# Optimization experiments

Hardware: AMD Instinct MI355X
Metric: run time of the kernel (lower is better)

Reference implementation:

```python
import jax, jax.numpy as jnp
import numpy as np

N_SUPPORT = 32768
N_QUERY = 16384
D = 512
K = 32
U = 128
NEG_BIG = -1e30  # masked-out attention logit; all-masked class -> uniform weights == mean fallback


def setup_inputs() -> dict:
    key = jax.random.key(0)
    k1, k2, k3, k4, k5 = jax.random.split(key, 5)
    query = jax.random.normal(k1, (N_QUERY, D), dtype=jnp.float32)
    support = jax.random.normal(k2, (N_SUPPORT, D), dtype=jnp.float32)
    labels = jax.random.randint(k3, (N_SUPPORT,), 0, K, dtype=jnp.int32)
    # Xavier-normal-ish init for per-class projection V (U,D) and attention vector w (U,1)
    V = jax.random.normal(k4, (K, U, D), dtype=jnp.float32) * np.float32(np.sqrt(2.0 / (U + D)))
    w = jax.random.normal(k5, (K, U), dtype=jnp.float32) * np.float32(np.sqrt(2.0 / (U + 1)))
    return {"query_embeddings": query, "support_embeddings": support,
            "support_labels": labels, "V": V, "w": w}


def reference(query_embeddings, support_embeddings, support_labels, V, w):
    # --- attention-weighted prototypes (vectorized over classes via masked softmax) ---
    # projected[k,n,u] = tanh(V[k] @ x_n)
    projected = jnp.tanh(jnp.einsum('nd,kud->knu', support_embeddings, V))
    attn_logits = jnp.einsum('knu,ku->kn', projected, w)              # (K, N)
    mask = support_labels[None, :] == jnp.arange(K, dtype=support_labels.dtype)[:, None]
    attn_logits = jnp.where(mask, attn_logits, NEG_BIG)
    # per-class softmax over support samples; an empty class yields uniform weights,
    # i.e. prototype = mean(embeddings) -- exactly the torch fallback branch.
    attn = jax.nn.softmax(attn_logits, axis=1)                        # (K, N)
    prototypes = jnp.einsum('kn,nd->kd', attn, support_embeddings)    # (K, D)

    # --- squared-euclidean distance classification ---
    q2 = jnp.sum(query_embeddings * query_embeddings, axis=1, keepdims=True)   # (B, 1)
    p2 = jnp.sum(prototypes * prototypes, axis=1)[None, :]                     # (1, K)
    dists = q2 + p2 - 2.0 * (query_embeddings @ prototypes.T)                  # (B, K)
    return jax.nn.log_softmax(-dists, axis=1)
```

## Files before the change

kernel.cpp:

```cpp
#include <hip/hip_runtime.h>
#include <hip/hip_bf16.h>

#define N_SUPPORT 32768
#define N_QUERY   16384
#define DIM       512
#define NCLS      32
#define NU        128
#define NBLK      (N_SUPPORT / 256)

#define OFF_IDX      0
#define OFF_COUNT    131072
#define OFF_START    131200
#define OFF_M        131456
#define OFF_Z        131584
#define OFF_P2       131712
#define OFF_LOGIT    132096
#define OFF_PRAW     263168
#define OFF_PROTO    328704
#define OFF_BHIST    394240
#define OFF_BOFFS    410624
#define OFF_VBF      458752
#define OFF_PBF      4653056

typedef __attribute__((ext_vector_type(8))) short short8;
typedef __attribute__((ext_vector_type(4))) short short4v;
typedef __attribute__((ext_vector_type(4))) float f32x4;

__device__ inline unsigned short f2bf(float f) {
    unsigned int x = __builtin_bit_cast(unsigned int, f);
    unsigned int r = x + 0x7fffu + ((x >> 16) & 1u);
    return (unsigned short)(r >> 16);
}
__device__ inline float bf2f(unsigned short h) {
    unsigned int u = ((unsigned int)h) << 16;
    return __builtin_bit_cast(float, u);
}

__device__ inline short8 pack_bf8(float4 f0, float4 f1) {
    short8 pk;
    pk[0] = f2bf(f0.x); pk[1] = f2bf(f0.y); pk[2] = f2bf(f0.z); pk[3] = f2bf(f0.w);
    pk[4] = f2bf(f1.x); pk[5] = f2bf(f1.y); pk[6] = f2bf(f1.z); pk[7] = f2bf(f1.w);
    return pk;
}

__device__ inline void pack_hilo(float4 f0, float4 f1, short8& hi, short8& lo) {
    float v[8] = {f0.x, f0.y, f0.z, f0.w, f1.x, f1.y, f1.z, f1.w};
    #pragma unroll
    for (int i = 0; i < 8; i++) {
        unsigned short h = f2bf(v[i]);
        hi[i] = (short)h;
        lo[i] = (short)f2bf(v[i] - bf2f(h));
    }
}

__global__ void k_vcast(const float* __restrict__ V, short* __restrict__ Vbf,
                        float* __restrict__ praw, const int* __restrict__ labels,
                        int* __restrict__ bhist) {
    __shared__ int h[NCLS];
    int tid = threadIdx.x;
    bool dohist = (blockIdx.x < NBLK);
    if (dohist) {
        if (tid < NCLS) h[tid] = 0;
        __syncthreads();
        atomicAdd(&h[labels[blockIdx.x * 256 + tid]], 1);
    }
    int i = blockIdx.x * 256 + tid;
    int ob = i * 4;
    int j0  = ob & 7;
    int s   = (ob >> 3) & 7;
    int u   = (ob >> 6) & 127;
    int c   = (ob >> 13) & 7;
    int k   = ob >> 16;
    int d   = c * 64 + ((s ^ (u & 7)) * 8) + j0;
    float4 f = *(const float4*)(V + ((size_t)(k * 128 + u) * DIM + d));
    short4v o;
    o[0] = f2bf(f.x); o[1] = f2bf(f.y); o[2] = f2bf(f.z); o[3] = f2bf(f.w);
    *(short4v*)(Vbf + (size_t)ob) = o;
    if (i < (NCLS * DIM) / 4) *(float4*)(praw + i * 4) = make_float4(0.f, 0.f, 0.f, 0.f);
    if (dohist) {
        __syncthreads();
        if (tid < NCLS) bhist[blockIdx.x * NCLS + tid] = h[tid];
    }
}

__global__ void k_scan2(const int* __restrict__ bhist, int* __restrict__ boffs,
                        int* __restrict__ start, int* __restrict__ count) {
    __shared__ int tot[NCLS];
    int tid = threadIdx.x;
    if (tid < NCLS) {
        int s = 0;
        for (int b = 0; b < NBLK; b++) {
            boffs[b * NCLS + tid] = s;
            s += bhist[b * NCLS + tid];
        }
        tot[tid] = s;
    }
    __syncthreads();
    if (tid == 0) {
        int run = 0;
        for (int k = 0; k < NCLS; k++) {
            start[k] = run;
            count[k] = tot[k];
            run += tot[k];
        }
        start[NCLS] = run;
    }
}

__global__ void k_scatter(const int* __restrict__ labels, const int* __restrict__ boffs,
                          const int* __restrict__ start, int* __restrict__ idx_c) {
    __shared__ int whist[4][NCLS];
    int tid = threadIdx.x;
    int n = blockIdx.x * 256 + tid;
    int l = labels[n];
    int lane = tid & 63, wid = tid >> 6;
    unsigned long long mymask = 0ull;
    #pragma unroll
    for (int k = 0; k < NCLS; k++) {
        unsigned long long mk = __ballot(l == k);
        if (k == l) mymask = mk;
        if (lane == k) whist[wid][k] = __popcll(mk);
    }
    int rank = __popcll(mymask & ((1ull << lane) - 1ull));
    __syncthreads();
    int wbase = 0;
    for (int w = 0; w < wid; w++) wbase += whist[w][l];
    idx_c[start[l] + boffs[blockIdx.x * NCLS + l] + wbase + rank] = n;
}

__launch_bounds__(512, 1)
__global__ void k_logits(const float* __restrict__ support, const short* __restrict__ Vbf,
                         const float* __restrict__ w, const int* __restrict__ idx_c,
                         const int* __restrict__ start, const int* __restrict__ count,
                         float* __restrict__ logit_c) {
    int k = blockIdx.y;
    int cnt = count[k];
    int base = blockIdx.x * 64;
    if (base >= cnt) return;
    int M = min(64, cnt - base);
    int s0 = start[k] + base;
    int t = threadIdx.x;

    __shared__ __align__(16) short Xs[2][64 * 64];
    __shared__ __align__(16) short Vs[2][128 * 64];
    __shared__ float part[8][64];
    __shared__ int sidx[64];
    if (t < 64) sidx[t] = idx_c[s0 + ((t < 64 && t < M) ? t : 0)];
    __syncthreads();

    int l = t & 63, wv = t >> 6;
    int lo16 = l & 15, hi4 = l >> 4;

    int xrow = t >> 3, xslot = t & 7;
    int xdst = xrow * 64 + ((xslot ^ (xrow & 7)) * 8);
    const float* xsrc = support + (size_t)sidx[xrow] * DIM + xslot * 8;
    const short* Vkc = Vbf + (size_t)k * (8 * 128 * 64);

    f32x4 acc[4];
    #pragma unroll
    for (int mt = 0; mt < 4; mt++) acc[mt] = (f32x4){0.f, 0.f, 0.f, 0.f};

    float4 xa0, xa1, xb0, xb1, xc0, xc1;
    short8 va[2], vb[2], vc[2];

#define LOADX(d0, d1, c) { d0 = *(const float4*)(xsrc + (c) * 64); \
                           d1 = *(const float4*)(xsrc + (c) * 64 + 4); }
#define LOADV(dst, c) { _Pragma("unroll") for (int rep = 0; rep < 2; rep++)   \
        dst[rep] = *(const short8*)(Vkc + (size_t)(c) * 8192 + (size_t)(t + 512 * rep) * 8); }
#define WRITEB(buf, x0, x1, vs) { *(short8*)&Xs[buf][xdst] = pack_bf8(x0, x1); \
        _Pragma("unroll") for (int rep = 0; rep < 2; rep++)                    \
        *(short8*)&Vs[buf][(t + 512 * rep) * 8] = vs[rep]; }
#define MFMA_CHUNK(cur) { _Pragma("unroll")                                       \
    for (int ks = 0; ks < 2; ks++) {                                              \
        short8 a[4], b;                                                           \
        _Pragma("unroll")                                                         \
        for (int mt = 0; mt < 4; mt++) {                                          \
            int ar = mt * 16 + lo16;                                              \
            a[mt] = *(short8*)&Xs[cur][ar * 64 + (((ks * 4 + hi4) ^ (ar & 7)) * 8)]; \
        }                                                                         \
        int vr = wv * 16 + lo16;                                                  \
        b = *(short8*)&Vs[cur][vr * 64 + (((ks * 4 + hi4) ^ (vr & 7)) * 8)];      \
        _Pragma("unroll")                                                         \
        for (int mt = 0; mt < 4; mt++)                                            \
            acc[mt] = __builtin_amdgcn_mfma_f32_16x16x32_bf16(a[mt], b, acc[mt], 0, 0, 0); \
    } }
#define BAR() { asm volatile("s_waitcnt lgkmcnt(0)" ::: "memory"); __builtin_amdgcn_s_barrier(); }

    LOADX(xa0, xa1, 0); LOADV(va, 0);
    LOADX(xb0, xb1, 1); LOADV(vb, 1);
    LOADX(xc0, xc1, 2); LOADV(vc, 2);
    WRITEB(0, xa0, xa1, va);

    BAR(); LOADX(xa0, xa1, 3); LOADV(va, 3); MFMA_CHUNK(0); WRITEB(1, xb0, xb1, vb);
    BAR(); LOADX(xb0, xb1, 4); LOADV(vb, 4); MFMA_CHUNK(1); WRITEB(0, xc0, xc1, vc);
    BAR(); LOADX(xc0, xc1, 5); LOADV(vc, 5); MFMA_CHUNK(0); WRITEB(1, xa0, xa1, va);
    BAR(); LOADX(xa0, xa1, 6); LOADV(va, 6); MFMA_CHUNK(1); WRITEB(0, xb0, xb1, vb);
    BAR(); LOADX(xb0, xb1, 7); LOADV(vb, 7); MFMA_CHUNK(0); WRITEB(1, xc0, xc1, vc);
    BAR(); MFMA_CHUNK(1); WRITEB(0, xa0, xa1, va);
    BAR(); MFMA_CHUNK(0); WRITEB(1, xb0, xb1, vb);
    BAR(); MFMA_CHUNK(1);

#undef LOADX
#undef LOADV
#undef WRITEB
#undef MFMA_CHUNK
#undef BAR

    float wval = w[k * NU + wv * 16 + lo16];
    #pragma unroll
    for (int mt = 0; mt < 4; mt++) {
        #pragma unroll
        for (int r = 0; r < 4; r++) {
            float val = tanhf(acc[mt][r]) * wval;
            val += __shfl_xor(val, 1);
            val += __shfl_xor(val, 2);
            val += __shfl_xor(val, 4);
            val += __shfl_xor(val, 8);
            if (lo16 == 0) part[wv][mt * 16 + hi4 * 4 + r] = val;
        }
    }
    __syncthreads();
    if (t < 64 && t < M) {
        float s = 0.f;
        #pragma unroll
        for (int wq = 0; wq < 8; wq++) s += part[wq][t];
        logit_c[s0 + t] = s;
    }
}

__global__ void k_mz(const float* __restrict__ logit_c, const int* __restrict__ start,
                     const int* __restrict__ count, float* __restrict__ m, float* __restrict__ Z) {
    int k = blockIdx.x;
    int cnt = count[k], s0 = start[k];
    int tid = threadIdx.x;
    __shared__ float red[256];
    float mx = -1e30f;
    for (int i = tid; i < cnt; i += 256) mx = fmaxf(mx, logit_c[s0 + i]);
    red[tid] = mx; __syncthreads();
    for (int off = 128; off > 0; off >>= 1) {
        if (tid < off) red[tid] = fmaxf(red[tid], red[tid + off]);
        __syncthreads();
    }
    float mk = red[0];
    __syncthreads();
    float s = 0.f;
    for (int i = tid; i < cnt; i += 256) s += expf(logit_c[s0 + i] - mk);
    red[tid] = s; __syncthreads();
    for (int off = 128; off > 0; off >>= 1) {
        if (tid < off) red[tid] += red[tid + off];
        __syncthreads();
    }
    if (tid == 0) { m[k] = mk; Z[k] = red[0]; }
}

__launch_bounds__(512, 1)
__global__ void k_proto(const float* __restrict__ support, const int* __restrict__ idx_c,
                        const float* __restrict__ logit_c, const int* __restrict__ start,
                        const int* __restrict__ count, const float* __restrict__ m,
                        float* __restrict__ praw) {
    int k = blockIdx.y;
    int cnt = count[k];
    int base = blockIdx.x * 64;
    if (base >= cnt) return;
    int M = min(64, cnt - base);
    int s0 = start[k] + base;
    __shared__ float wts[64];
    __shared__ int sid[64];
    int t = threadIdx.x;
    if (t < 64) {
        sid[t] = idx_c[s0 + ((t < M) ? t : 0)];
        wts[t] = (t < M) ? expf(logit_c[s0 + t] - m[k]) : 0.f;
    }
    __syncthreads();
    int d = t;
    float a = 0.f;
    for (int s = 0; s < 64; s += 4) {
        float r0 = support[(size_t)sid[s + 0] * DIM + d];
        float r1 = support[(size_t)sid[s + 1] * DIM + d];
        float r2 = support[(size_t)sid[s + 2] * DIM + d];
        float r3 = support[(size_t)sid[s + 3] * DIM + d];
        a += wts[s] * r0 + wts[s + 1] * r1 + wts[s + 2] * r2 + wts[s + 3] * r3;
    }
    atomicAdd(&praw[k * DIM + d], a);
}

__global__ void k_protonorm(const float* __restrict__ support, const float* __restrict__ praw,
                            const float* __restrict__ Z, const int* __restrict__ count,
                            float* __restrict__ proto, float* __restrict__ p2,
                            short* __restrict__ Pbf) {
    int k = blockIdx.x;
    int tid = threadIdx.x;
    int cnt = count[k];
    __shared__ float red[256];
    float pv[2];
    if (cnt > 0) {
        float inv = 1.f / Z[k];
        #pragma unroll
        for (int i = 0; i < 2; i++) pv[i] = praw[k * DIM + tid + i * 256] * inv;
    } else {
        #pragma unroll
        for (int i = 0; i < 2; i++) {
            int d = tid + i * 256;
            float s = 0.f;
            for (int n = 0; n < N_SUPPORT; n++) s += support[(size_t)n * DIM + d];
            pv[i] = s * (1.f / N_SUPPORT);
        }
    }
    float acc = 0.f;
    #pragma unroll
    for (int i = 0; i < 2; i++) {
        int d = tid + i * 256;
        proto[k * DIM + d] = pv[i];
        acc += pv[i] * pv[i];
        int c = d >> 6, off = d & 63, o = off >> 3, j = off & 7;
        int s = o ^ (k & 7);
        int pos = (c * 32 + k) * 64 + s * 8 + j;
        unsigned short hi = f2bf(pv[i]);
        Pbf[pos] = (short)hi;
        Pbf[NCLS * DIM + pos] = (short)f2bf(pv[i] - bf2f(hi));
    }
    red[tid] = acc; __syncthreads();
    for (int off = 128; off > 0; off >>= 1) {
        if (tid < off) red[tid] += red[tid + off];
        __syncthreads();
    }
    if (tid == 0) p2[k] = red[0];
}

__launch_bounds__(256, 1)
__global__ void k_dist(const float* __restrict__ query, const short* __restrict__ Pbf,
                       const float* __restrict__ p2, float* __restrict__ out) {
    __shared__ __align__(16) short Ph[NCLS * DIM];
    __shared__ __align__(16) short Pl[NCLS * DIM];
    __shared__ __align__(16) short Qh[2][64 * 64];
    __shared__ __align__(16) short Ql[2][64 * 64];
    int t = threadIdx.x;
    int qbase = blockIdx.x * 64;
    int l = t & 63, wv = t >> 6;
    int lo16 = l & 15, hi4 = l >> 4;

    #pragma unroll
    for (int rep = 0; rep < 8; rep++) {
        int u = t + 256 * rep;
        ((short8*)Ph)[u] = ((const short8*)Pbf)[u];
        ((short8*)Pl)[u] = ((const short8*)(Pbf + NCLS * DIM))[u];
    }

    int qrow[2], qslot[2], qdst[2];
    const float* qsrc[2];
    #pragma unroll
    for (int rep = 0; rep < 2; rep++) {
        int u = t + 256 * rep;
        qrow[rep] = u >> 3; qslot[rep] = u & 7;
        qdst[rep] = qrow[rep] * 64 + ((qslot[rep] ^ (qrow[rep] & 7)) * 8);
        qsrc[rep] = query + (size_t)(qbase + qrow[rep]) * DIM + qslot[rep] * 8;
    }

    f32x4 acc[2];
    acc[0] = (f32x4){0.f, 0.f, 0.f, 0.f};
    acc[1] = (f32x4){0.f, 0.f, 0.f, 0.f};

    float4 qa[2][2], qb[2][2];
#define LOADQ(d, c) { _Pragma("unroll") for (int rep = 0; rep < 2; rep++) { \
        d[rep][0] = *(const float4*)(qsrc[rep] + (c) * 64);                 \
        d[rep][1] = *(const float4*)(qsrc[rep] + (c) * 64 + 4); } }
#define WRITEQ(buf, d) { _Pragma("unroll") for (int rep = 0; rep < 2; rep++) { \
        short8 hi8, lo8;                                                        \
        pack_hilo(d[rep][0], d[rep][1], hi8, lo8);                              \
        *(short8*)&Qh[buf][qdst[rep]] = hi8;                                    \
        *(short8*)&Ql[buf][qdst[rep]] = lo8; } }

    LOADQ(qa, 0);
    LOADQ(qb, 1);
    WRITEQ(0, qa);

    for (int c = 0; c < 8; ++c) {
        int cur = c & 1;
        __syncthreads();
        if (c + 2 < 8) {
            if (cur == 0) { LOADQ(qa, c + 2); }
            else          { LOADQ(qb, c + 2); }
        }
        #pragma unroll
        for (int ks = 0; ks < 2; ks++) {
            int arow = wv * 16 + lo16;
            int asw = ((ks * 4 + hi4) ^ (arow & 7)) * 8;
            short8 ah = *(short8*)&Qh[cur][arow * 64 + asw];
            short8 al = *(short8*)&Ql[cur][arow * 64 + asw];
            #pragma unroll
            for (int nt = 0; nt < 2; nt++) {
                int brow = nt * 16 + lo16;
                int pos = (c * 32 + brow) * 64 + (((ks * 4 + hi4) ^ (brow & 7)) * 8);
                short8 bh = *(short8*)&Ph[pos];
                short8 bl = *(short8*)&Pl[pos];
                acc[nt] = __builtin_amdgcn_mfma_f32_16x16x32_bf16(ah, bh, acc[nt], 0, 0, 0);
                acc[nt] = __builtin_amdgcn_mfma_f32_16x16x32_bf16(ah, bl, acc[nt], 0, 0, 0);
                acc[nt] = __builtin_amdgcn_mfma_f32_16x16x32_bf16(al, bh, acc[nt], 0, 0, 0);
            }
        }
        if (c < 7) {
            if (cur == 0) { WRITEQ(1, qb); }
            else          { WRITEQ(0, qa); }
        }
    }
#undef LOADQ
#undef WRITEQ

    float p2v0 = p2[lo16];
    float p2v1 = p2[16 + lo16];
    #pragma unroll
    for (int r = 0; r < 4; r++) {
        float l0 = 2.f * acc[0][r] - p2v0;
        float l1 = 2.f * acc[1][r] - p2v1;
        float mx = fmaxf(l0, l1);
        mx = fmaxf(mx, __shfl_xor(mx, 1));
        mx = fmaxf(mx, __shfl_xor(mx, 2));
        mx = fmaxf(mx, __shfl_xor(mx, 4));
        mx = fmaxf(mx, __shfl_xor(mx, 8));
        float s = expf(l0 - mx) + expf(l1 - mx);
        s += __shfl_xor(s, 1);
        s += __shfl_xor(s, 2);
        s += __shfl_xor(s, 4);
        s += __shfl_xor(s, 8);
        float lse = mx + logf(s);
        int q = qbase + wv * 16 + hi4 * 4 + r;
        out[(size_t)q * NCLS + lo16] = l0 - lse;
        out[(size_t)q * NCLS + 16 + lo16] = l1 - lse;
    }
}

extern "C" void kernel_launch(void* const* d_in, const int* in_sizes, int n_in,
                              void* d_out, int out_size, void* d_ws, size_t ws_size,
                              hipStream_t stream) {
    const float* query   = (const float*)d_in[0];
    const float* support = (const float*)d_in[1];
    const int*   labels  = (const int*)d_in[2];
    const float* V       = (const float*)d_in[3];
    const float* w       = (const float*)d_in[4];
    float* out = (float*)d_out;
    char* ws = (char*)d_ws;

    int*   idx_c   = (int*)(ws + OFF_IDX);
    int*   count   = (int*)(ws + OFF_COUNT);
    int*   start   = (int*)(ws + OFF_START);
    float* m       = (float*)(ws + OFF_M);
    float* Z       = (float*)(ws + OFF_Z);
    float* p2      = (float*)(ws + OFF_P2);
    float* logit_c = (float*)(ws + OFF_LOGIT);
    float* praw    = (float*)(ws + OFF_PRAW);
    float* proto   = (float*)(ws + OFF_PROTO);
    int*   bhist   = (int*)(ws + OFF_BHIST);
    int*   boffs   = (int*)(ws + OFF_BOFFS);
    short* vbf     = (short*)(ws + OFF_VBF);
    short* pbf     = (short*)(ws + OFF_PBF);

    hipLaunchKernelGGL(k_vcast, dim3((NCLS * NU * DIM) / 1024), dim3(256), 0, stream,
                       V, vbf, praw, labels, bhist);
    hipLaunchKernelGGL(k_scan2, dim3(1), dim3(64), 0, stream, bhist, boffs, start, count);
    hipLaunchKernelGGL(k_scatter, dim3(NBLK), dim3(256), 0, stream, labels, boffs, start, idx_c);
    hipLaunchKernelGGL(k_logits, dim3(32, NCLS), dim3(512), 0, stream,
                       support, vbf, w, idx_c, start, count, logit_c);
    hipLaunchKernelGGL(k_mz, dim3(NCLS), dim3(256), 0, stream, logit_c, start, count, m, Z);
    hipLaunchKernelGGL(k_proto, dim3(32, NCLS), dim3(512), 0, stream,
                       support, idx_c, logit_c, start, count, m, praw);
    hipLaunchKernelGGL(k_protonorm, dim3(NCLS), dim3(256), 0, stream,
                       support, praw, Z, count, proto, p2, pbf);
    hipLaunchKernelGGL(k_dist, dim3(N_QUERY / 64), dim3(256), 0, stream, query, pbf, p2, out);
}
```

Before: 70.61 us.

## Use direct global-to-LDS loads for V with smaller 32-row logits tiles

The per-class logits GEMM kernel is restructured from 512-thread blocks over 64 support rows, with a register-staged triple-buffered pipeline, to 256-thread blocks over 32 rows. V chunks are now copied straight into LDS with global_load_lds, and each wave computes a 2x2 set of MFMA tiles. The aims are to raise block count and occupancy and to cut register pressure and VGPR staging of V. In exchange, V is fetched twice as often in total, and the single-buffered loop exposes load latency behind two barriers per chunk.

```diff
diff --git a/kernel.cpp b/kernel.cpp
--- a/kernel.cpp
+++ b/kernel.cpp
@@ -25,6 +25,9 @@
 typedef __attribute__((ext_vector_type(8))) short short8;
 typedef __attribute__((ext_vector_type(4))) short short4v;
 typedef __attribute__((ext_vector_type(4))) float f32x4;
+
+typedef __attribute__((address_space(3))) unsigned int lds_u32;
+typedef const __attribute__((address_space(1))) unsigned int glb_u32;
 
 __device__ inline unsigned short f2bf(float f) {
     unsigned int x = __builtin_bit_cast(unsigned int, f);
@@ -128,24 +131,24 @@
     idx_c[start[l] + boffs[blockIdx.x * NCLS + l] + wbase + rank] = n;
 }
 
-__launch_bounds__(512, 1)
+__launch_bounds__(256, 1)
 __global__ void k_logits(const float* __restrict__ support, const short* __restrict__ Vbf,
                          const float* __restrict__ w, const int* __restrict__ idx_c,
                          const int* __restrict__ start, const int* __restrict__ count,
                          float* __restrict__ logit_c) {
     int k = blockIdx.y;
     int cnt = count[k];
-    int base = blockIdx.x * 64;
+    int base = blockIdx.x * 32;
     if (base >= cnt) return;
-    int M = min(64, cnt - base);
+    int M = min(32, cnt - base);
     int s0 = start[k] + base;
     int t = threadIdx.x;
 
-    __shared__ __align__(16) short Xs[2][64 * 64];
-    __shared__ __align__(16) short Vs[2][128 * 64];
-    __shared__ float part[8][64];
-    __shared__ int sidx[64];
-    if (t < 64) sidx[t] = idx_c[s0 + ((t < 64 && t < M) ? t : 0)];
+    __shared__ __align__(16) short Xs[32 * 64];
+    __shared__ __align__(16) short Vs[128 * 64];
+    __shared__ float part[4][32];
+    __shared__ int sidx[32];
+    if (t < 32) sidx[t] = idx_c[s0 + ((t < M) ? t : 0)];
     __syncthreads();
 
     int l = t & 63, wv = t >> 6;
@@ -156,62 +159,58 @@
     const float* xsrc = support + (size_t)sidx[xrow] * DIM + xslot * 8;
     const short* Vkc = Vbf + (size_t)k * (8 * 128 * 64);
 
-    f32x4 acc[4];
-    #pragma unroll
-    for (int mt = 0; mt < 4; mt++) acc[mt] = (f32x4){0.f, 0.f, 0.f, 0.f};
-
-    float4 xa0, xa1, xb0, xb1, xc0, xc1;
-    short8 va[2], vb[2], vc[2];
-
-#define LOADX(d0, d1, c) { d0 = *(const float4*)(xsrc + (c) * 64); \
-                           d1 = *(const float4*)(xsrc + (c) * 64 + 4); }
-#define LOADV(dst, c) { _Pragma("unroll") for (int rep = 0; rep < 2; rep++)   \
-        dst[rep] = *(const short8*)(Vkc + (size_t)(c) * 8192 + (size_t)(t + 512 * rep) * 8); }
-#define WRITEB(buf, x0, x1, vs) { *(short8*)&Xs[buf][xdst] = pack_bf8(x0, x1); \
-        _Pragma("unroll") for (int rep = 0; rep < 2; rep++)                    \
-        *(short8*)&Vs[buf][(t + 512 * rep) * 8] = vs[rep]; }
-#define MFMA_CHUNK(cur) { _Pragma("unroll")                                       \
-    for (int ks = 0; ks < 2; ks++) {                                              \
-        short8 a[4], b;                                                           \
-        _Pragma("unroll")                                                         \
-        for (int mt = 0; mt < 4; mt++) {                                          \
-            int ar = mt * 16 + lo16;                                              \
-            a[mt] = *(short8*)&Xs[cur][ar * 64 + (((ks * 4 + hi4) ^ (ar & 7)) * 8)]; \
-        }                                                                         \
-        int vr = wv * 16 + lo16;                                                  \
-        b = *(short8*)&Vs[cur][vr * 64 + (((ks * 4 + hi4) ^ (vr & 7)) * 8)];      \
-        _Pragma("unroll")                                                         \
-        for (int mt = 0; mt < 4; mt++)                                            \
-            acc[mt] = __builtin_amdgcn_mfma_f32_16x16x32_bf16(a[mt], b, acc[mt], 0, 0, 0); \
-    } }
-#define BAR() { asm volatile("s_waitcnt lgkmcnt(0)" ::: "memory"); __builtin_amdgcn_s_barrier(); }
-
-    LOADX(xa0, xa1, 0); LOADV(va, 0);
-    LOADX(xb0, xb1, 1); LOADV(vb, 1);
-    LOADX(xc0, xc1, 2); LOADV(vc, 2);
-    WRITEB(0, xa0, xa1, va);
-
-    BAR(); LOADX(xa0, xa1, 3); LOADV(va, 3); MFMA_CHUNK(0); WRITEB(1, xb0, xb1, vb);
-    BAR(); LOADX(xb0, xb1, 4); LOADV(vb, 4); MFMA_CHUNK(1); WRITEB(0, xc0, xc1, vc);
-    BAR(); LOADX(xc0, xc1, 5); LOADV(vc, 5); MFMA_CHUNK(0); WRITEB(1, xa0, xa1, va);
-    BAR(); LOADX(xa0, xa1, 6); LOADV(va, 6); MFMA_CHUNK(1); WRITEB(0, xb0, xb1, vb);
-    BAR(); LOADX(xb0, xb1, 7); LOADV(vb, 7); MFMA_CHUNK(0); WRITEB(1, xc0, xc1, vc);
-    BAR(); MFMA_CHUNK(1); WRITEB(0, xa0, xa1, va);
-    BAR(); MFMA_CHUNK(0); WRITEB(1, xb0, xb1, vb);
-    BAR(); MFMA_CHUNK(1);
-
-#undef LOADX
-#undef LOADV
-#undef WRITEB
-#undef MFMA_CHUNK
-#undef BAR
-
-    float wval = w[k * NU + wv * 16 + lo16];
-    #pragma unroll
-    for (int mt = 0; mt < 4; mt++) {
+    f32x4 acc[2][2];
+    #pragma unroll
+    for (int mt = 0; mt < 2; mt++)
+        #pragma unroll
+        for (int nt = 0; nt < 2; nt++) acc[mt][nt] = (f32x4){0.f, 0.f, 0.f, 0.f};
+
+    float4 xv0 = *(const float4*)(xsrc);
+    float4 xv1 = *(const float4*)(xsrc + 4);
+
+    for (int c = 0; c < 8; ++c) {
+        __syncthreads();
+        #pragma unroll
+        for (int rep = 0; rep < 4; rep++) {
+            int u = t + 256 * rep;
+            __builtin_amdgcn_global_load_lds(
+                (glb_u32*)(Vkc + (size_t)c * 8192 + (size_t)u * 8),
+                (lds_u32*)&Vs[u * 8], 16, 0, 0);
+        }
+        *(short8*)&Xs[xdst] = pack_bf8(xv0, xv1);
+        __syncthreads();
+        if (c < 7) {
+            xv0 = *(const float4*)(xsrc + (c + 1) * 64);
+            xv1 = *(const float4*)(xsrc + (c + 1) * 64 + 4);
+        }
+        #pragma unroll
+        for (int ks = 0; ks < 2; ks++) {
+            short8 a[2], b[2];
+            #pragma unroll
+            for (int mt = 0; mt < 2; mt++) {
+                int ar = mt * 16 + lo16;
+                a[mt] = *(short8*)&Xs[ar * 64 + (((ks * 4 + hi4) ^ (ar & 7)) * 8)];
+            }
+            #pragma unroll
+            for (int nt = 0; nt < 2; nt++) {
+                int vr = wv * 32 + nt * 16 + lo16;
+                b[nt] = *(short8*)&Vs[vr * 64 + (((ks * 4 + hi4) ^ (vr & 7)) * 8)];
+            }
+            #pragma unroll
+            for (int mt = 0; mt < 2; mt++)
+                #pragma unroll
+                for (int nt = 0; nt < 2; nt++)
+                    acc[mt][nt] = __builtin_amdgcn_mfma_f32_16x16x32_bf16(a[mt], b[nt], acc[mt][nt], 0, 0, 0);
+        }
+    }
+
+    float w0 = w[k * NU + wv * 32 + lo16];
+    float w1 = w[k * NU + wv * 32 + 16 + lo16];
+    #pragma unroll
+    for (int mt = 0; mt < 2; mt++) {
         #pragma unroll
         for (int r = 0; r < 4; r++) {
-            float val = tanhf(acc[mt][r]) * wval;
+            float val = tanhf(acc[mt][0][r]) * w0 + tanhf(acc[mt][1][r]) * w1;
             val += __shfl_xor(val, 1);
             val += __shfl_xor(val, 2);
             val += __shfl_xor(val, 4);
@@ -220,11 +219,8 @@
         }
     }
     __syncthreads();
-    if (t < 64 && t < M) {
-        float s = 0.f;
-        #pragma unroll
-        for (int wq = 0; wq < 8; wq++) s += part[wq][t];
-        logit_c[s0 + t] = s;
+    if (t < M) {
+        logit_c[s0 + t] = part[0][t] + part[1][t] + part[2][t] + part[3][t];
     }
 }
 
@@ -458,7 +454,7 @@
                        V, vbf, praw, labels, bhist);
     hipLaunchKernelGGL(k_scan2, dim3(1), dim3(64), 0, stream, bhist, boffs, start, count);
     hipLaunchKernelGGL(k_scatter, dim3(NBLK), dim3(256), 0, stream, labels, boffs, start, idx_c);
-    hipLaunchKernelGGL(k_logits, dim3(32, NCLS), dim3(512), 0, stream,
+    hipLaunchKernelGGL(k_logits, dim3(64, NCLS), dim3(256), 0, stream,
                        support, vbf, w, idx_c, start, count, logit_c);
     hipLaunchKernelGGL(k_mz, dim3(NCLS), dim3(256), 0, stream, logit_c, start, count, m, Z);
     hipLaunchKernelGGL(k_proto, dim3(32, NCLS), dim3(512), 0, stream,
```

Result: slower. 73.50 us (+4.1%).
